# Kernel optimization log

Measured on AMD Instinct MI355X. Metric: run time of the kernel, lower is better.

Reference implementation:

```python
import jax, jax.numpy as jnp
import numpy as np

D_MODEL = 64
N_HEAD = 4
HEAD_DIM = D_MODEL // N_HEAD  # 16


def setup_inputs() -> dict:
    key = jax.random.key(0)
    ks = jax.random.split(key, 8)
    B, T_dec, T_enc = 16, 1024, 1024
    s = 1.0 / np.sqrt(D_MODEL)
    return {
        "x": jax.random.normal(ks[0], (B, T_dec, D_MODEL), dtype=jnp.float32),
        "encoder_outputs": jax.random.normal(ks[1], (B, T_enc, D_MODEL), dtype=jnp.float32),
        "encoder_outputs_mask": jnp.ones((B, T_enc), dtype=jnp.int32),
        "Wkv": jax.random.normal(ks[2], (D_MODEL, 2 * D_MODEL), dtype=jnp.float32) * s,
        "bkv": jnp.zeros((2 * D_MODEL,), dtype=jnp.float32),
        "Wq": jax.random.normal(ks[3], (D_MODEL, D_MODEL), dtype=jnp.float32) * s,
        "bq": jnp.zeros((D_MODEL,), dtype=jnp.float32),
        "Wproj": jax.random.normal(ks[4], (D_MODEL, D_MODEL), dtype=jnp.float32) * s,
        "bproj": jnp.zeros((D_MODEL,), dtype=jnp.float32),
    }


def reference(x, encoder_outputs, encoder_outputs_mask, Wkv, bkv, Wq, bq, Wproj, bproj):
    B, T_dec, C = x.shape
    T_enc = encoder_outputs.shape[1]
    kv = encoder_outputs @ Wkv + bkv                      # [B, T_enc, 2C]
    k, v = kv[..., :D_MODEL], kv[..., D_MODEL:]          # [B, T_enc, C]
    q = x @ Wq + bq                                      # [B, T_dec, C]
    q = q.reshape(B, T_dec, N_HEAD, HEAD_DIM)
    k = k.reshape(B, T_enc, N_HEAD, HEAD_DIM)
    v = v.reshape(B, T_enc, N_HEAD, HEAD_DIM)
    scale = 1.0 / jnp.sqrt(jnp.asarray(HEAD_DIM, dtype=q.dtype))
    att = jnp.einsum("bqhd,bkhd->bhqk", q, k) * scale    # [B, H, T_dec, T_enc]
    mask = (encoder_outputs_mask == 0)[:, None, None, :]  # [B, 1, 1, T_enc]
    att = jnp.where(mask, jnp.asarray(-jnp.inf, dtype=att.dtype), att)
    att = jax.nn.softmax(att, axis=-1)
    ctx = jnp.einsum("bhqk,bkhd->bqhd", att, v).reshape(B, T_dec, C)
    # dropout is identity at eval time
    return ctx @ Wproj + bproj
```

## Files before the change

### kernel.cpp

```cpp
#include <hip/hip_runtime.h>
#include <hip/hip_bf16.h>
#include <math.h>

#define DM 64
#define NH 4
#define HD 16
#define BATCH 16
#define TSEQ 1024

typedef short bf16x8 __attribute__((ext_vector_type(8)));
typedef short bf16x4 __attribute__((ext_vector_type(4)));
typedef float f32x4  __attribute__((ext_vector_type(4)));
typedef float f32x16 __attribute__((ext_vector_type(16)));

static __device__ inline short f2bf(float x) {
    __hip_bfloat16 h = __float2bfloat16(x);
    return __builtin_bit_cast(short, h);
}
static __device__ inline float bf2f(short s) {
    __hip_bfloat16 h = __builtin_bit_cast(__hip_bfloat16, s);
    return __bfloat162float(h);
}

__global__ __launch_bounds__(256) void proj_kernel(
    const float* __restrict__ x, const float* __restrict__ enc,
    const float* __restrict__ Wkv, const float* __restrict__ bkv,
    const float* __restrict__ Wq,  const float* __restrict__ bq,
    const int* __restrict__ mask,
    short* __restrict__ qhi, short* __restrict__ qlo,
    short* __restrict__ khi, short* __restrict__ klo,
    short* __restrict__ vtt)
{
    const int t = threadIdx.x;
    const int part = blockIdx.y;
    const int r = blockIdx.x * 256 + t;
    const int b = r >> 10, trow = r & 1023;

    const float* in; const float* W; const float* bias; int cb, ldw;
    if (part < 4)      { in = x;   W = Wq;  ldw = 64;  cb = part*16;          bias = bq;  }
    else if (part < 8) { in = enc; W = Wkv; ldw = 128; cb = (part-4)*16;      bias = bkv; }
    else               { in = enc; W = Wkv; ldw = 128; cb = 64 + (part-8)*16; bias = bkv; }

    __shared__ float wsl[64][16];
    for (int idx = t; idx < 1024; idx += 256)
        wsl[idx >> 4][idx & 15] = W[(idx >> 4)*ldw + cb + (idx & 15)];

    float4 xr[16];
    const float4* inrow = (const float4*)(in + (size_t)r * 64);
    #pragma unroll
    for (int i = 0; i < 16; ++i) xr[i] = inrow[i];
    __syncthreads();

    float acc[16];
    #pragma unroll
    for (int j = 0; j < 16; ++j) acc[j] = bias[cb + j];
    #pragma unroll
    for (int k = 0; k < 64; ++k) {
        const float xv = ((const float*)xr)[k];
        const float4 w0 = ((const float4*)&wsl[k][0])[0];
        const float4 w1 = ((const float4*)&wsl[k][0])[1];
        const float4 w2 = ((const float4*)&wsl[k][0])[2];
        const float4 w3 = ((const float4*)&wsl[k][0])[3];
        acc[0]  += xv*w0.x; acc[1]  += xv*w0.y; acc[2]  += xv*w0.z; acc[3]  += xv*w0.w;
        acc[4]  += xv*w1.x; acc[5]  += xv*w1.y; acc[6]  += xv*w1.z; acc[7]  += xv*w1.w;
        acc[8]  += xv*w2.x; acc[9]  += xv*w2.y; acc[10] += xv*w2.z; acc[11] += xv*w2.w;
        acc[12] += xv*w3.x; acc[13] += xv*w3.y; acc[14] += xv*w3.z; acc[15] += xv*w3.w;
    }

    if (part < 8) {
        const float scale = (part < 4) ? 0.36067376022224085f : 1.0f;
        short* dh = (part < 4) ? qhi : khi;
        short* dl = (part < 4) ? qlo : klo;
        const int h = (part < 4) ? part : (part - 4);
        bf16x8 h0, h1, l0, l1;
        #pragma unroll
        for (int j = 0; j < 16; ++j) {
            float vf = acc[j] * scale;
            short hb = f2bf(vf);
            short lb = f2bf(vf - bf2f(hb));
            if (j < 8) { h0[j] = hb; l0[j] = lb; }
            else       { h1[j-8] = hb; l1[j-8] = lb; }
        }
        size_t off = (((size_t)(b*NH + h))*TSEQ + trow)*HD;
        *(bf16x8*)(dh + off)     = h0;
        *(bf16x8*)(dh + off + 8) = h1;
        *(bf16x8*)(dl + off)     = l0;
        *(bf16x8*)(dl + off + 8) = l1;
    } else {
        const int h = part - 8;
        const float mb = (mask[b*TSEQ + trow] != 0) ? 1.0f : 0.0f;
        short* tile = vtt + ((size_t)(b*NH + h))*32768 + (size_t)(trow >> 5)*1024;
        const int kw = trow & 31;
        #pragma unroll
        for (int j = 0; j < 16; ++j)
            tile[j*32 + kw] = f2bf(acc[j] * mb);
        tile[16*32 + kw] = (mb != 0.0f) ? (short)0x3F80 : (short)0;
    }
}

__global__ __launch_bounds__(512) void attn_kernel(
    const short* __restrict__ qhi, const short* __restrict__ qlo,
    const short* __restrict__ khi, const short* __restrict__ klo,
    const short* __restrict__ vtt,
    const float* __restrict__ Wproj, const float* __restrict__ bproj,
    float* __restrict__ out)
{
    const int tid  = threadIdx.x;
    const int lane = tid & 63;
    const int wid  = __builtin_amdgcn_readfirstlane(tid >> 6);
    const int h  = wid & 3;
    const int ks = wid >> 2;
    const int qbase = blockIdx.x * 32;
    const int b  = blockIdx.y;
    const int l31 = lane & 31, half = lane >> 5;

    __shared__ short Pb[8][32][36];
    __shared__ float Cbuf[2][32][67];
    __shared__ float Lbuf[2][NH][32];

    const size_t qoff = (((size_t)(b*NH + h))*TSEQ + qbase + l31)*HD + half*8;
    const bf16x8 qAh = *(const bf16x8*)(qhi + qoff);
    const bf16x8 qAl = *(const bf16x8*)(qlo + qoff);

    const short* khb = khi + (((size_t)(b*NH + h))*TSEQ + ks*512)*HD;
    const short* klb = klo + (((size_t)(b*NH + h))*TSEQ + ks*512)*HD;
    const short* vtb = vtt + ((size_t)(b*NH + h))*32768 + (size_t)ks*16384;

    f32x16 Cacc;
    #pragma unroll
    for (int i = 0; i < 16; ++i) Cacc[i] = 0.f;

    short* pw = &Pb[wid][0][0];
    const short* pr = &Pb[wid][l31][0];

    for (int step = 0; step < 16; ++step) {
        const int ko = step * 32;
        const bf16x8 kBh = *(const bf16x8*)(khb + (size_t)(ko + l31)*HD + half*8);
        const bf16x8 kBl = *(const bf16x8*)(klb + (size_t)(ko + l31)*HD + half*8);
        const short* tile = vtb + (size_t)step * 1024;
        const bf16x8 vB0 = *(const bf16x8*)(tile + l31*32 + half*8);
        const bf16x8 vB1 = *(const bf16x8*)(tile + l31*32 + 16 + half*8);

        f32x16 S;
        #pragma unroll
        for (int i = 0; i < 16; ++i) S[i] = 0.f;
        S = __builtin_amdgcn_mfma_f32_32x32x16_bf16(qAh, kBh, S, 0, 0, 0);
        S = __builtin_amdgcn_mfma_f32_32x32x16_bf16(qAh, kBl, S, 0, 0, 0);
        S = __builtin_amdgcn_mfma_f32_32x32x16_bf16(qAl, kBh, S, 0, 0, 0);

        #pragma unroll
        for (int i = 0; i < 16; ++i) {
            const float p = __builtin_amdgcn_exp2f(S[i]);
            const int row = (i & 3) + 8*(i >> 2) + 4*half;
            pw[row*36 + l31] = f2bf(p);
        }

        const bf16x4 a0 = *(const bf16x4*)(pr + half*8);
        const bf16x4 a1 = *(const bf16x4*)(pr + half*8 + 4);
        const bf16x4 a2 = *(const bf16x4*)(pr + 16 + half*8);
        const bf16x4 a3 = *(const bf16x4*)(pr + 16 + half*8 + 4);
        const bf16x8 pA0 = __builtin_shufflevector(a0, a1, 0, 1, 2, 3, 4, 5, 6, 7);
        const bf16x8 pA1 = __builtin_shufflevector(a2, a3, 0, 1, 2, 3, 4, 5, 6, 7);

        Cacc = __builtin_amdgcn_mfma_f32_32x32x16_bf16(pA0, vB0, Cacc, 0, 0, 0);
        Cacc = __builtin_amdgcn_mfma_f32_32x32x16_bf16(pA1, vB1, Cacc, 0, 0, 0);
    }

    #pragma unroll
    for (int r = 0; r < 16; ++r) {
        const int row = (r & 3) + 8*(r >> 2) + 4*half;
        if (l31 < 16)        Cbuf[ks][row][h*HD + l31] = Cacc[r];
        else if (l31 == 16)  Lbuf[ks][h][row] = Cacc[r];
    }
    __syncthreads();

    const int q   = tid >> 4;
    const int cbo = (tid & 15) * 4;
    float linv[NH];
    #pragma unroll
    for (int hh = 0; hh < NH; ++hh)
        linv[hh] = 1.0f / (Lbuf[0][hh][q] + Lbuf[1][hh][q]);

    float o0 = bproj[cbo], o1 = bproj[cbo+1], o2 = bproj[cbo+2], o3 = bproj[cbo+3];
    #pragma unroll
    for (int i = 0; i < 64; ++i) {
        const float cv = (Cbuf[0][q][i] + Cbuf[1][q][i]) * linv[i >> 4];
        const float4 wr = *(const float4*)(Wproj + i*DM + cbo);
        o0 += cv*wr.x; o1 += cv*wr.y; o2 += cv*wr.z; o3 += cv*wr.w;
    }
    float4 st; st.x = o0; st.y = o1; st.z = o2; st.w = o3;
    *(float4*)(out + ((size_t)b*TSEQ + qbase + q)*DM + cbo) = st;
}

extern "C" void kernel_launch(void* const* d_in, const int* in_sizes, int n_in,
                              void* d_out, int out_size, void* d_ws, size_t ws_size,
                              hipStream_t stream) {
    const float* x     = (const float*)d_in[0];
    const float* enc   = (const float*)d_in[1];
    const int*   mask  = (const int*)  d_in[2];
    const float* Wkv   = (const float*)d_in[3];
    const float* bkv   = (const float*)d_in[4];
    const float* Wq    = (const float*)d_in[5];
    const float* bq    = (const float*)d_in[6];
    const float* Wproj = (const float*)d_in[7];
    const float* bproj = (const float*)d_in[8];
    float* out = (float*)d_out;

    const size_t SZ = (size_t)BATCH*NH*TSEQ*HD;
    short* qhi = (short*)d_ws;
    short* qlo = qhi + SZ;
    short* khi = qlo + SZ;
    short* klo = khi + SZ;
    short* vtt = klo + SZ;

    proj_kernel<<<dim3(64, 12), dim3(256), 0, stream>>>(
        x, enc, Wkv, bkv, Wq, bq, mask, qhi, qlo, khi, klo, vtt);
    attn_kernel<<<dim3(32, 16), dim3(512), 0, stream>>>(
        qhi, qlo, khi, klo, vtt, Wproj, bproj, out);
}
```

Baseline: 112.9 us.

## Transpose attention MFMAs to keep P in registers and double rows per thread in projection

The attention kernel swaps the MFMA operand order to compute S^T = K·Q^T and ctx^T = V^T·P^T. The probability tile then stays in registers and only needs a cross-half lane shuffle, instead of a round trip through LDS. Separately, the projection kernel makes each thread handle two rows with chunked, prefetched input loads, halving the grid and reusing each LDS weight read. This removes LDS traffic from the inner attention loop, at the cost of more register pressure and lane shuffles.

New measurement: 114.3 us. No clear change (+1.2%).

```diff
diff --git a/kernel.cpp b/kernel.cpp
--- a/kernel.cpp
+++ b/kernel.cpp
@@ -9,8 +9,6 @@
 #define TSEQ 1024
 
 typedef short bf16x8 __attribute__((ext_vector_type(8)));
-typedef short bf16x4 __attribute__((ext_vector_type(4)));
-typedef float f32x4  __attribute__((ext_vector_type(4)));
 typedef float f32x16 __attribute__((ext_vector_type(16)));
 
 static __device__ inline short f2bf(float x) {
@@ -20,6 +18,11 @@
 static __device__ inline float bf2f(short s) {
     __hip_bfloat16 h = __builtin_bit_cast(__hip_bfloat16, s);
     return __bfloat162float(h);
+}
+static __device__ inline unsigned pack2bf(float a, float b) {
+    const unsigned lo = (unsigned short)f2bf(a);
+    const unsigned hi = (unsigned short)f2bf(b);
+    return lo | (hi << 16);
 }
 
 __global__ __launch_bounds__(256) void proj_kernel(
@@ -33,68 +36,94 @@
 {
     const int t = threadIdx.x;
     const int part = blockIdx.y;
-    const int r = blockIdx.x * 256 + t;
-    const int b = r >> 10, trow = r & 1023;
+    const int r0 = blockIdx.x * 512 + t;
 
     const float* in; const float* W; const float* bias; int cb, ldw;
     if (part < 4)      { in = x;   W = Wq;  ldw = 64;  cb = part*16;          bias = bq;  }
     else if (part < 8) { in = enc; W = Wkv; ldw = 128; cb = (part-4)*16;      bias = bkv; }
     else               { in = enc; W = Wkv; ldw = 128; cb = 64 + (part-8)*16; bias = bkv; }
 
+    const float4* row0 = (const float4*)(in + (size_t)r0 * 64);
+    const float4* row1 = (const float4*)(in + (size_t)(r0 + 256) * 64);
+
+    float4 xc[2][4];
+    #pragma unroll
+    for (int v4 = 0; v4 < 4; ++v4) { xc[0][v4] = row0[v4]; xc[1][v4] = row1[v4]; }
+
     __shared__ float wsl[64][16];
+    #pragma unroll
     for (int idx = t; idx < 1024; idx += 256)
         wsl[idx >> 4][idx & 15] = W[(idx >> 4)*ldw + cb + (idx & 15)];
-
-    float4 xr[16];
-    const float4* inrow = (const float4*)(in + (size_t)r * 64);
-    #pragma unroll
-    for (int i = 0; i < 16; ++i) xr[i] = inrow[i];
     __syncthreads();
 
-    float acc[16];
-    #pragma unroll
-    for (int j = 0; j < 16; ++j) acc[j] = bias[cb + j];
-    #pragma unroll
-    for (int k = 0; k < 64; ++k) {
-        const float xv = ((const float*)xr)[k];
-        const float4 w0 = ((const float4*)&wsl[k][0])[0];
-        const float4 w1 = ((const float4*)&wsl[k][0])[1];
-        const float4 w2 = ((const float4*)&wsl[k][0])[2];
-        const float4 w3 = ((const float4*)&wsl[k][0])[3];
-        acc[0]  += xv*w0.x; acc[1]  += xv*w0.y; acc[2]  += xv*w0.z; acc[3]  += xv*w0.w;
-        acc[4]  += xv*w1.x; acc[5]  += xv*w1.y; acc[6]  += xv*w1.z; acc[7]  += xv*w1.w;
-        acc[8]  += xv*w2.x; acc[9]  += xv*w2.y; acc[10] += xv*w2.z; acc[11] += xv*w2.w;
-        acc[12] += xv*w3.x; acc[13] += xv*w3.y; acc[14] += xv*w3.z; acc[15] += xv*w3.w;
-    }
-
-    if (part < 8) {
-        const float scale = (part < 4) ? 0.36067376022224085f : 1.0f;
-        short* dh = (part < 4) ? qhi : khi;
-        short* dl = (part < 4) ? qlo : klo;
-        const int h = (part < 4) ? part : (part - 4);
-        bf16x8 h0, h1, l0, l1;
-        #pragma unroll
-        for (int j = 0; j < 16; ++j) {
-            float vf = acc[j] * scale;
-            short hb = f2bf(vf);
-            short lb = f2bf(vf - bf2f(hb));
-            if (j < 8) { h0[j] = hb; l0[j] = lb; }
-            else       { h1[j-8] = hb; l1[j-8] = lb; }
-        }
-        size_t off = (((size_t)(b*NH + h))*TSEQ + trow)*HD;
-        *(bf16x8*)(dh + off)     = h0;
-        *(bf16x8*)(dh + off + 8) = h1;
-        *(bf16x8*)(dl + off)     = l0;
-        *(bf16x8*)(dl + off + 8) = l1;
-    } else {
-        const int h = part - 8;
-        const float mb = (mask[b*TSEQ + trow] != 0) ? 1.0f : 0.0f;
-        short* tile = vtt + ((size_t)(b*NH + h))*32768 + (size_t)(trow >> 5)*1024;
-        const int kw = trow & 31;
-        #pragma unroll
-        for (int j = 0; j < 16; ++j)
-            tile[j*32 + kw] = f2bf(acc[j] * mb);
-        tile[16*32 + kw] = (mb != 0.0f) ? (short)0x3F80 : (short)0;
+    float acc[2][16];
+    #pragma unroll
+    for (int j = 0; j < 16; ++j) { float bj = bias[cb + j]; acc[0][j] = bj; acc[1][j] = bj; }
+
+    for (int kc = 0; kc < 4; ++kc) {
+        float4 xn[2][4];
+        if (kc < 3) {
+            #pragma unroll
+            for (int v4 = 0; v4 < 4; ++v4) {
+                xn[0][v4] = row0[(kc+1)*4 + v4];
+                xn[1][v4] = row1[(kc+1)*4 + v4];
+            }
+        }
+        #pragma unroll
+        for (int i = 0; i < 16; ++i) {
+            const int k = kc*16 + i;
+            const float4 w0 = ((const float4*)&wsl[k][0])[0];
+            const float4 w1 = ((const float4*)&wsl[k][0])[1];
+            const float4 w2 = ((const float4*)&wsl[k][0])[2];
+            const float4 w3 = ((const float4*)&wsl[k][0])[3];
+            #pragma unroll
+            for (int rr = 0; rr < 2; ++rr) {
+                const float xv = ((const float*)&xc[rr][i >> 2])[i & 3];
+                acc[rr][0]  += xv*w0.x; acc[rr][1]  += xv*w0.y; acc[rr][2]  += xv*w0.z; acc[rr][3]  += xv*w0.w;
+                acc[rr][4]  += xv*w1.x; acc[rr][5]  += xv*w1.y; acc[rr][6]  += xv*w1.z; acc[rr][7]  += xv*w1.w;
+                acc[rr][8]  += xv*w2.x; acc[rr][9]  += xv*w2.y; acc[rr][10] += xv*w2.z; acc[rr][11] += xv*w2.w;
+                acc[rr][12] += xv*w3.x; acc[rr][13] += xv*w3.y; acc[rr][14] += xv*w3.z; acc[rr][15] += xv*w3.w;
+            }
+        }
+        if (kc < 3) {
+            #pragma unroll
+            for (int v4 = 0; v4 < 4; ++v4) { xc[0][v4] = xn[0][v4]; xc[1][v4] = xn[1][v4]; }
+        }
+    }
+
+    #pragma unroll
+    for (int rr = 0; rr < 2; ++rr) {
+        const int r = r0 + rr*256;
+        const int b = r >> 10, trow = r & 1023;
+        if (part < 8) {
+            const float scale = (part < 4) ? 0.36067376022224085f : 1.0f;
+            short* dh = (part < 4) ? qhi : khi;
+            short* dl = (part < 4) ? qlo : klo;
+            const int h = (part < 4) ? part : (part - 4);
+            bf16x8 h0, h1, l0, l1;
+            #pragma unroll
+            for (int j = 0; j < 16; ++j) {
+                float vf = acc[rr][j] * scale;
+                short hb = f2bf(vf);
+                short lb = f2bf(vf - bf2f(hb));
+                if (j < 8) { h0[j] = hb; l0[j] = lb; }
+                else       { h1[j-8] = hb; l1[j-8] = lb; }
+            }
+            size_t off = (((size_t)(b*NH + h))*TSEQ + trow)*HD;
+            *(bf16x8*)(dh + off)     = h0;
+            *(bf16x8*)(dh + off + 8) = h1;
+            *(bf16x8*)(dl + off)     = l0;
+            *(bf16x8*)(dl + off + 8) = l1;
+        } else {
+            const int h = part - 8;
+            const float mb = (mask[b*TSEQ + trow] != 0) ? 1.0f : 0.0f;
+            short* tile = vtt + ((size_t)(b*NH + h))*32768 + (size_t)(trow >> 5)*1024;
+            const int kw = trow & 31;
+            #pragma unroll
+            for (int j = 0; j < 16; ++j)
+                tile[j*32 + kw] = f2bf(acc[rr][j] * mb);
+            tile[16*32 + kw] = (mb != 0.0f) ? (short)0x3F80 : (short)0;
+        }
     }
 }
 
@@ -112,15 +141,15 @@
     const int ks = wid >> 2;
     const int qbase = blockIdx.x * 32;
     const int b  = blockIdx.y;
-    const int l31 = lane & 31, half = lane >> 5;
-
-    __shared__ short Pb[8][32][36];
+    const int l31 = lane & 31;
+    const bool hf = (lane >> 5) != 0;
+
     __shared__ float Cbuf[2][32][67];
     __shared__ float Lbuf[2][NH][32];
 
-    const size_t qoff = (((size_t)(b*NH + h))*TSEQ + qbase + l31)*HD + half*8;
-    const bf16x8 qAh = *(const bf16x8*)(qhi + qoff);
-    const bf16x8 qAl = *(const bf16x8*)(qlo + qoff);
+    const size_t qoff = (((size_t)(b*NH + h))*TSEQ + qbase + l31)*HD + (hf ? 8 : 0);
+    const bf16x8 qBh = *(const bf16x8*)(qhi + qoff);
+    const bf16x8 qBl = *(const bf16x8*)(qlo + qoff);
 
     const short* khb = khi + (((size_t)(b*NH + h))*TSEQ + ks*512)*HD;
     const short* klb = klo + (((size_t)(b*NH + h))*TSEQ + ks*512)*HD;
@@ -130,48 +159,60 @@
     #pragma unroll
     for (int i = 0; i < 16; ++i) Cacc[i] = 0.f;
 
-    short* pw = &Pb[wid][0][0];
-    const short* pr = &Pb[wid][l31][0];
-
     for (int step = 0; step < 16; ++step) {
         const int ko = step * 32;
-        const bf16x8 kBh = *(const bf16x8*)(khb + (size_t)(ko + l31)*HD + half*8);
-        const bf16x8 kBl = *(const bf16x8*)(klb + (size_t)(ko + l31)*HD + half*8);
+        const bf16x8 kAh = *(const bf16x8*)(khb + (size_t)(ko + l31)*HD + (hf ? 8 : 0));
+        const bf16x8 kAl = *(const bf16x8*)(klb + (size_t)(ko + l31)*HD + (hf ? 8 : 0));
         const short* tile = vtb + (size_t)step * 1024;
-        const bf16x8 vB0 = *(const bf16x8*)(tile + l31*32 + half*8);
-        const bf16x8 vB1 = *(const bf16x8*)(tile + l31*32 + 16 + half*8);
+        const bf16x8 vA0 = *(const bf16x8*)(tile + l31*32 + (hf ? 8 : 0));
+        const bf16x8 vA1 = *(const bf16x8*)(tile + l31*32 + 16 + (hf ? 8 : 0));
 
         f32x16 S;
         #pragma unroll
         for (int i = 0; i < 16; ++i) S[i] = 0.f;
-        S = __builtin_amdgcn_mfma_f32_32x32x16_bf16(qAh, kBh, S, 0, 0, 0);
-        S = __builtin_amdgcn_mfma_f32_32x32x16_bf16(qAh, kBl, S, 0, 0, 0);
-        S = __builtin_amdgcn_mfma_f32_32x32x16_bf16(qAl, kBh, S, 0, 0, 0);
-
-        #pragma unroll
-        for (int i = 0; i < 16; ++i) {
-            const float p = __builtin_amdgcn_exp2f(S[i]);
-            const int row = (i & 3) + 8*(i >> 2) + 4*half;
-            pw[row*36 + l31] = f2bf(p);
-        }
-
-        const bf16x4 a0 = *(const bf16x4*)(pr + half*8);
-        const bf16x4 a1 = *(const bf16x4*)(pr + half*8 + 4);
-        const bf16x4 a2 = *(const bf16x4*)(pr + 16 + half*8);
-        const bf16x4 a3 = *(const bf16x4*)(pr + 16 + half*8 + 4);
-        const bf16x8 pA0 = __builtin_shufflevector(a0, a1, 0, 1, 2, 3, 4, 5, 6, 7);
-        const bf16x8 pA1 = __builtin_shufflevector(a2, a3, 0, 1, 2, 3, 4, 5, 6, 7);
-
-        Cacc = __builtin_amdgcn_mfma_f32_32x32x16_bf16(pA0, vB0, Cacc, 0, 0, 0);
-        Cacc = __builtin_amdgcn_mfma_f32_32x32x16_bf16(pA1, vB1, Cacc, 0, 0, 0);
-    }
-
-    #pragma unroll
-    for (int r = 0; r < 16; ++r) {
-        const int row = (r & 3) + 8*(r >> 2) + 4*half;
-        if (l31 < 16)        Cbuf[ks][row][h*HD + l31] = Cacc[r];
-        else if (l31 == 16)  Lbuf[ks][h][row] = Cacc[r];
-    }
+        S = __builtin_amdgcn_mfma_f32_32x32x16_bf16(kAh, qBh, S, 0, 0, 0);
+        S = __builtin_amdgcn_mfma_f32_32x32x16_bf16(kAh, qBl, S, 0, 0, 0);
+        S = __builtin_amdgcn_mfma_f32_32x32x16_bf16(kAl, qBh, S, 0, 0, 0);
+
+        float p[16];
+        #pragma unroll
+        for (int i = 0; i < 16; ++i) p[i] = __builtin_amdgcn_exp2f(S[i]);
+
+        unsigned pk[8];
+        #pragma unroll
+        for (int i = 0; i < 8; ++i) pk[i] = pack2bf(p[2*i], p[2*i+1]);
+
+        const unsigned sA = hf ? pk[0] : pk[2];
+        const unsigned sB = hf ? pk[1] : pk[3];
+        const unsigned sC = hf ? pk[4] : pk[6];
+        const unsigned sD = hf ? pk[5] : pk[7];
+        const unsigned rA = (unsigned)__shfl_xor((int)sA, 32);
+        const unsigned rB = (unsigned)__shfl_xor((int)sB, 32);
+        const unsigned rC = (unsigned)__shfl_xor((int)sC, 32);
+        const unsigned rD = (unsigned)__shfl_xor((int)sD, 32);
+
+        int4 b1, b2;
+        b1.x = hf ? (int)rA    : (int)pk[0];
+        b1.y = hf ? (int)rB    : (int)pk[1];
+        b1.z = hf ? (int)pk[2] : (int)rA;
+        b1.w = hf ? (int)pk[3] : (int)rB;
+        b2.x = hf ? (int)rC    : (int)pk[4];
+        b2.y = hf ? (int)rD    : (int)pk[5];
+        b2.z = hf ? (int)pk[6] : (int)rC;
+        b2.w = hf ? (int)pk[7] : (int)rD;
+        const bf16x8 pB0 = __builtin_bit_cast(bf16x8, b1);
+        const bf16x8 pB1 = __builtin_bit_cast(bf16x8, b2);
+
+        Cacc = __builtin_amdgcn_mfma_f32_32x32x16_bf16(vA0, pB0, Cacc, 0, 0, 0);
+        Cacc = __builtin_amdgcn_mfma_f32_32x32x16_bf16(vA1, pB1, Cacc, 0, 0, 0);
+    }
+
+    #pragma unroll
+    for (int r = 0; r < 8; ++r) {
+        const int d = (r & 3) + 8*(r >> 2) + (hf ? 4 : 0);
+        Cbuf[ks][l31][h*HD + d] = Cacc[r];
+    }
+    if (!hf) Lbuf[ks][h][l31] = Cacc[8];
     __syncthreads();
 
     const int q   = tid >> 4;
@@ -213,7 +254,7 @@
     short* klo = khi + SZ;
     short* vtt = klo + SZ;
 
-    proj_kernel<<<dim3(64, 12), dim3(256), 0, stream>>>(
+    proj_kernel<<<dim3(32, 12), dim3(256), 0, stream>>>(
         x, enc, Wkv, bkv, Wq, bq, mask, qhi, qlo, khi, klo, vtt);
     attn_kernel<<<dim3(32, 16), dim3(512), 0, stream>>>(
         qhi, qlo, khi, klo, vtt, Wproj, bproj, out);
```
